# Optimization experiments

Measured on AMD Instinct MI355X. Metric: run time of the kernel, lower is better.

Reference implementation:

```python
import jax, jax.numpy as jnp
import numpy as np

N_NODES = 100000
N_EDGES = 1280000
IN_DIM = 64
HID = 64
OUT_DIM = 2
N_GRAPHS = 1000
BN_EPS = 1e-5


def setup_inputs() -> dict:
    key = jax.random.key(0)
    ks = jax.random.split(key, 16)
    x = jax.random.normal(ks[0], (N_NODES, IN_DIM), dtype=jnp.float32)
    edge_index = jax.random.randint(ks[1], (2, N_EDGES), 0, N_NODES, dtype=jnp.int64)
    batch = jnp.sort(jax.random.randint(ks[2], (N_NODES,), 0, N_GRAPHS, dtype=jnp.int64))
    # He-init linear weights (stored as [in, out] so forward is x @ W)
    def he(k, fan_in, fan_out):
        return jax.random.normal(k, (fan_in, fan_out), dtype=jnp.float32) * np.sqrt(2.0 / fan_in)
    return {
        "x": x,
        "edge_index": edge_index,
        "batch": batch,
        "bn_in_g": jnp.ones((IN_DIM,), jnp.float32),
        "bn_in_b": jnp.zeros((IN_DIM,), jnp.float32),
        "W1": he(ks[3], IN_DIM, HID), "b1": jnp.zeros((HID,), jnp.float32),
        "g1": jnp.ones((HID,), jnp.float32), "be1": jnp.zeros((HID,), jnp.float32),
        "W2": he(ks[4], HID, HID), "b2": jnp.zeros((HID,), jnp.float32),
        "g2": jnp.ones((HID,), jnp.float32), "be2": jnp.zeros((HID,), jnp.float32),
        "Wout": he(ks[5], HID, OUT_DIM), "bout": jnp.zeros((OUT_DIM,), jnp.float32),
    }


def _batchnorm(x, g, b):
    # training-mode BN over the node dimension (biased variance, as torch uses for normalization)
    m = jnp.mean(x, axis=0)
    v = jnp.mean(jnp.square(x - m), axis=0)
    return (x - m) * jax.lax.rsqrt(v + BN_EPS) * g + b


def _gcn_norm(edge_index, n):
    # PyG GCNConv normalization with added self-loops:
    # norm_e = deg[src]^-1/2 * deg[dst]^-1/2, deg computed on A + I over targets.
    row = jnp.concatenate([edge_index[0], jnp.arange(n, dtype=edge_index.dtype)])
    col = jnp.concatenate([edge_index[1], jnp.arange(n, dtype=edge_index.dtype)])
    deg = jax.ops.segment_sum(jnp.ones_like(col, dtype=jnp.float32), col, num_segments=n)
    dinv = jnp.where(deg > 0, jax.lax.rsqrt(deg), 0.0)
    norm = dinv[row] * dinv[col]
    return row, col, norm


def _gcn_conv(x, W, b, row, col, norm, n):
    h = x @ W                                   # [N, out]
    msg = h[row] * norm[:, None]                # gather over edges (incl. self-loops)
    agg = jax.ops.segment_sum(msg, col, num_segments=n)
    return agg + b


def reference(x, edge_index, batch, bn_in_g, bn_in_b, W1, b1, g1, be1, W2, b2, g2, be2, Wout, bout):
    n = x.shape[0]
    row, col, norm = _gcn_norm(edge_index, n)
    h = _batchnorm(x, bn_in_g, bn_in_b)         # input BN (dropout = identity in eval)
    h = _gcn_conv(h, W1, b1, row, col, norm, n)
    h = _batchnorm(jax.nn.relu(h), g1, be1)
    h = _gcn_conv(h, W2, b2, row, col, norm, n)
    h = _batchnorm(jax.nn.relu(h), g2, be2)
    # global mean pool per graph
    sums = jax.ops.segment_sum(h, batch, num_segments=N_GRAPHS)
    cnts = jax.ops.segment_sum(jnp.ones((n,), h.dtype), batch, num_segments=N_GRAPHS)
    pooled = sums / jnp.maximum(cnts, 1.0)[:, None]
    return pooled @ Wout + bout                 # [N_GRAPHS, OUT_DIM]
```

## Files before the change

### kernel.cpp

```cpp
#include <hip/hip_runtime.h>
#include <math.h>

#define N_NODES 100000
#define N_EDGES 1280000
#define DIM 64
#define N_GRAPHS 1000
#define BN_EPS 1e-5f
#define NB 392
#define P1B 256
#define P1E 5000
#define SB 400
#define WIN 128
#define NWIN (N_EDGES / WIN)
#define GU 8
#define NSLOT 32

__device__ __forceinline__ unsigned int bf16_rtn2(float a, float b) {
    unsigned int ua = __float_as_uint(a);
    unsigned int ub = __float_as_uint(b);
    ua = (ua + 0x7FFFu + ((ua >> 16) & 1u)) >> 16;
    ub = (ub + 0x7FFFu + ((ub >> 16) & 1u)) >> 16;
    return ua | (ub << 16);
}
__device__ __forceinline__ unsigned short bf16r(float a) {
    unsigned int u = __float_as_uint(a);
    return (unsigned short)((u + 0x7FFFu + ((u >> 16) & 1u)) >> 16);
}
__device__ __forceinline__ float bfup(unsigned short u) {
    return __uint_as_float(((unsigned int)u) << 16);
}

__global__ __launch_bounds__(256) void k_p1hist(const int* __restrict__ ei,
                                                const int* __restrict__ batch,
                                                const float* __restrict__ X,
                                                int* __restrict__ bh,
                                                int* __restrict__ start,
                                                float* __restrict__ gsum,
                                                float* __restrict__ gsumsq) {
    int t = threadIdx.x;
    if (blockIdx.x < P1B) {
        __shared__ int hist[NB];
        for (int b = t; b < NB; b += 256) hist[b] = 0;
        __syncthreads();
        int e0 = blockIdx.x * P1E;
        #pragma unroll 4
        for (int e = e0 + t; e < e0 + P1E; e += 256)
            atomicAdd(&hist[ei[N_EDGES + e] >> 8], 1);
        __syncthreads();
        for (int b = t; b < NB; b += 256) bh[b * P1B + blockIdx.x] = hist[b];
    } else if (blockIdx.x < P1B + SB) {
        int grp = blockIdx.x - P1B;
        int j = t & 63, rg = t >> 6;
        int base = grp * 250;
        float s = 0.f, s2 = 0.f;
        for (int i = base + rg; i < base + 250; i += 4) {
            float v = X[i * DIM + j];
            s += v; s2 += v * v;
        }
        __shared__ float ls[256], ls2[256];
        ls[t] = s; ls2[t] = s2;
        __syncthreads();
        if (t < 64) {
            int slot = (grp & (NSLOT - 1)) * DIM;
            s  = ls[j]  + ls[64 + j]  + ls[128 + j]  + ls[192 + j];
            s2 = ls2[j] + ls2[64 + j] + ls2[128 + j] + ls2[192 + j];
            atomicAdd(&gsum[slot + j], s);
            atomicAdd(&gsumsq[slot + j], s2);
        }
    } else {
        int i = (blockIdx.x - P1B - SB) * 256 + t;
        if (i < N_NODES) {
            int cur = batch[i];
            if (i == 0) { for (int q = 0; q <= cur; q++) start[q] = 0; }
            else {
                int prev = batch[i - 1];
                for (int q = prev + 1; q <= cur; q++) start[q] = i;
            }
            if (i == N_NODES - 1)
                for (int q = cur + 1; q <= N_GRAPHS; q++) start[q] = N_NODES;
        }
    }
}

__global__ void k_scan1(const int* __restrict__ bh, int* __restrict__ iscan,
                        int* __restrict__ bsum) {
    __shared__ int ls[256];
    int i = blockIdx.x * 256 + threadIdx.x;
    int v = bh[i];
    ls[threadIdx.x] = v;
    __syncthreads();
    for (int off = 1; off < 256; off <<= 1) {
        int tv = (threadIdx.x >= off) ? ls[threadIdx.x - off] : 0;
        __syncthreads();
        ls[threadIdx.x] += tv;
        __syncthreads();
    }
    iscan[i] = ls[threadIdx.x];
    if (threadIdx.x == 255) bsum[blockIdx.x] = ls[255];
}

__global__ void k_scan2(const int* __restrict__ bsum, int* __restrict__ boff) {
    __shared__ int ls[512];
    int t = threadIdx.x;
    int v0 = (t < NB) ? bsum[t] : 0;
    ls[t] = v0;
    __syncthreads();
    for (int off = 1; off < 512; off <<= 1) {
        int v = (t >= off) ? ls[t - off] : 0;
        __syncthreads();
        ls[t] += v;
        __syncthreads();
    }
    if (t < NB) boff[t] = ls[t] - v0;
}

__global__ __launch_bounds__(256) void k_p1scat(const int* __restrict__ ei,
                                                const int* __restrict__ bh,
                                                const int* __restrict__ iscan,
                                                const int* __restrict__ boff,
                                                int2* __restrict__ tmp) {
    __shared__ int cur[NB];
    int blk = blockIdx.x;
    for (int b = threadIdx.x; b < NB; b += 256) {
        int i = b * P1B + blk;
        cur[b] = boff[b] + iscan[i] - bh[i];
    }
    __syncthreads();
    int e0 = blk * P1E;
    for (int e = e0 + threadIdx.x; e < e0 + P1E; e += 256) {
        int r = ei[e], c = ei[N_EDGES + e];
        int pos = atomicAdd(&cur[c >> 8], 1);
        tmp[pos] = make_int2(r, c);
    }
}

__global__ __launch_bounds__(256) void k_p2a(const int2* __restrict__ tmp,
                                             const int* __restrict__ bh,
                                             const int* __restrict__ iscan,
                                             const int* __restrict__ boff,
                                             int* __restrict__ rowstart,
                                             float* __restrict__ dinv,
                                             int* __restrict__ winnode) {
    int b = blockIdx.x, t = threadIdx.x;
    int bstart = boff[b] + iscan[b * 256] - bh[b * 256];
    int bend = (b == NB - 1) ? N_EDGES
                             : (boff[b + 1] + iscan[(b + 1) * 256] - bh[(b + 1) * 256]);
    __shared__ int cnt[256], scn[256];
    cnt[t] = 0;
    __syncthreads();
    for (int e = bstart + t; e < bend; e += 256)
        atomicAdd(&cnt[tmp[e].y & 255], 1);
    __syncthreads();
    scn[t] = cnt[t];
    __syncthreads();
    for (int off = 1; off < 256; off <<= 1) {
        int v = (t >= off) ? scn[t - off] : 0;
        __syncthreads();
        scn[t] += v;
        __syncthreads();
    }
    int node = b * 256 + t;
    int rs = bstart + scn[t] - cnt[t];
    if (node <= N_NODES) rowstart[node] = rs;
    if (node < N_NODES) {
        int deg = cnt[t];
        dinv[node] = 1.0f / sqrtf((float)(deg + 1));
        int re = rs + deg;
        for (int w = (rs + WIN - 1) / WIN; w * WIN < re; ++w) winnode[w] = node;
    }
}

__global__ __launch_bounds__(256) void k_p2b(const int2* __restrict__ tmp,
                                             const int* __restrict__ bh,
                                             const int* __restrict__ iscan,
                                             const int* __restrict__ boff,
                                             const int* __restrict__ rowstart,
                                             const float* __restrict__ dinv,
                                             int2* __restrict__ csr_ew) {
    int b = blockIdx.x, t = threadIdx.x;
    int bstart = boff[b] + iscan[b * 256] - bh[b * 256];
    int bend = (b == NB - 1) ? N_EDGES
                             : (boff[b + 1] + iscan[(b + 1) * 256] - bh[(b + 1) * 256]);
    __shared__ int curs[256];
    __shared__ float dl[256];
    int node = b * 256 + t;
    curs[t] = (node < N_NODES) ? rowstart[node] : 0;
    dl[t]   = (node < N_NODES) ? dinv[node] : 0.f;
    __syncthreads();
    for (int e = bstart + t; e < bend; e += 256) {
        int2 rec = tmp[e];
        int ld = rec.y & 255;
        int pos = atomicAdd(&curs[ld], 1);
        float w = dl[ld] * dinv[rec.x];
        csr_ew[pos] = make_int2(rec.x, (int)__float_as_uint(w));
    }
}

__global__ void k_bnfold(float* __restrict__ gsum, float* __restrict__ gsumsq,
                         const float* __restrict__ g, const float* __restrict__ b,
                         const float* __restrict__ W,
                         float* __restrict__ scale, float* __restrict__ cshift) {
    int j = threadIdx.x;
    float ms = 0.f, m2 = 0.f;
    for (int k = 0; k < NSLOT; k++) {
        ms += gsum[k * DIM + j];   gsum[k * DIM + j] = 0.f;
        m2 += gsumsq[k * DIM + j]; gsumsq[k * DIM + j] = 0.f;
    }
    float mean = ms * (1.0f / N_NODES);
    float var  = m2 * (1.0f / N_NODES) - mean * mean;
    float inv  = 1.0f / sqrtf(var + BN_EPS);
    float sc   = g[j] * inv;
    scale[j] = sc;
    __shared__ float shl[64];
    shl[j] = b[j] - mean * sc;
    __syncthreads();
    float s = 0.f;
    for (int k = 0; k < DIM; k++) s += shl[k] * W[k * DIM + j];
    cshift[j] = s;
}

__global__ void k_bnfinal(const float* __restrict__ gsum, const float* __restrict__ gsumsq,
                          const float* __restrict__ g, const float* __restrict__ b,
                          float* __restrict__ scale, float* __restrict__ shift) {
    int j = threadIdx.x;
    float ms = 0.f, m2 = 0.f;
    for (int k = 0; k < NSLOT; k++) { ms += gsum[k * DIM + j]; m2 += gsumsq[k * DIM + j]; }
    float mean = ms * (1.0f / N_NODES);
    float var  = m2 * (1.0f / N_NODES) - mean * mean;
    float inv  = 1.0f / sqrtf(var + BN_EPS);
    float sc   = g[j] * inv;
    scale[j] = sc;
    shift[j] = b[j] - mean * sc;
}

__global__ __launch_bounds__(256) void k_gemm_f32(const float* __restrict__ X,
                                                  const float* __restrict__ W,
                                                  const float* __restrict__ scale,
                                                  const float* __restrict__ cshift,
                                                  unsigned short* __restrict__ T) {
    __shared__ float Wl[64 * 64];
    __shared__ float Al[64 * 65];
    for (int t = threadIdx.x; t < 4096; t += 256) {
        int k = t >> 6;
        Wl[t] = W[t] * scale[k];
    }
    int row0 = blockIdx.x * 64;
    for (int t = threadIdx.x; t < 4096; t += 256) {
        int r = t >> 6, k = t & 63;
        int i = row0 + r;
        Al[r * 65 + k] = (i < N_NODES) ? X[(size_t)i * DIM + k] : 0.f;
    }
    __syncthreads();
    int r = threadIdx.x & 63;
    int q = threadIdx.x >> 6;
    float acc[16];
    #pragma unroll
    for (int jj = 0; jj < 16; jj++) acc[jj] = cshift[q * 16 + jj];
    #pragma unroll 4
    for (int k = 0; k < 64; k++) {
        float a = Al[r * 65 + k];
        const float4* wv = (const float4*)&Wl[k * 64 + q * 16];
        float4 w0 = wv[0], w1 = wv[1], w2 = wv[2], w3 = wv[3];
        acc[0]  += a * w0.x; acc[1]  += a * w0.y; acc[2]  += a * w0.z; acc[3]  += a * w0.w;
        acc[4]  += a * w1.x; acc[5]  += a * w1.y; acc[6]  += a * w1.z; acc[7]  += a * w1.w;
        acc[8]  += a * w2.x; acc[9]  += a * w2.y; acc[10] += a * w2.z; acc[11] += a * w2.w;
        acc[12] += a * w3.x; acc[13] += a * w3.y; acc[14] += a * w3.z; acc[15] += a * w3.w;
    }
    int i = row0 + r;
    if (i < N_NODES) {
        unsigned int pk[8];
        #pragma unroll
        for (int jj = 0; jj < 8; jj++) pk[jj] = bf16_rtn2(acc[2 * jj], acc[2 * jj + 1]);
        uint4* outv = (uint4*)&T[(size_t)i * DIM + q * 16];
        outv[0] = make_uint4(pk[0], pk[1], pk[2], pk[3]);
        outv[1] = make_uint4(pk[4], pk[5], pk[6], pk[7]);
    }
}

__global__ __launch_bounds__(256) void k_gemm_b16(const unsigned short* __restrict__ X,
                                                  const float* __restrict__ W,
                                                  const float* __restrict__ scale,
                                                  const float* __restrict__ cshift,
                                                  unsigned short* __restrict__ T) {
    __shared__ float Wl[64 * 64];
    __shared__ float Al[64 * 65];
    for (int t = threadIdx.x; t < 4096; t += 256) {
        int k = t >> 6;
        Wl[t] = W[t] * scale[k];
    }
    int row0 = blockIdx.x * 64;
    for (int t = threadIdx.x; t < 4096; t += 256) {
        int r = t >> 6, k = t & 63;
        int i = row0 + r;
        Al[r * 65 + k] = (i < N_NODES) ? bfup(X[(size_t)i * DIM + k]) : 0.f;
    }
    __syncthreads();
    int r = threadIdx.x & 63;
    int q = threadIdx.x >> 6;
    float acc[16];
    #pragma unroll
    for (int jj = 0; jj < 16; jj++) acc[jj] = cshift[q * 16 + jj];
    #pragma unroll 4
    for (int k = 0; k < 64; k++) {
        float a = Al[r * 65 + k];
        const float4* wv = (const float4*)&Wl[k * 64 + q * 16];
        float4 w0 = wv[0], w1 = wv[1], w2 = wv[2], w3 = wv[3];
        acc[0]  += a * w0.x; acc[1]  += a * w0.y; acc[2]  += a * w0.z; acc[3]  += a * w0.w;
        acc[4]  += a * w1.x; acc[5]  += a * w1.y; acc[6]  += a * w1.z; acc[7]  += a * w1.w;
        acc[8]  += a * w2.x; acc[9]  += a * w2.y; acc[10] += a * w2.z; acc[11] += a * w2.w;
        acc[12] += a * w3.x; acc[13] += a * w3.y; acc[14] += a * w3.z; acc[15] += a * w3.w;
    }
    int i = row0 + r;
    if (i < N_NODES) {
        unsigned int pk[8];
        #pragma unroll
        for (int jj = 0; jj < 8; jj++) pk[jj] = bf16_rtn2(acc[2 * jj], acc[2 * jj + 1]);
        uint4* outv = (uint4*)&T[(size_t)i * DIM + q * 16];
        outv[0] = make_uint4(pk[0], pk[1], pk[2], pk[3]);
        outv[1] = make_uint4(pk[4], pk[5], pk[6], pk[7]);
    }
}

__global__ __launch_bounds__(256) void k_zstrad(const int* __restrict__ rowstart,
                                                const int* __restrict__ winnode,
                                                float* __restrict__ C) {
    int lane = threadIdx.x & 63;
    int w = blockIdx.x * 4 + (threadIdx.x >> 6);
    int n = winnode[w];
    if (rowstart[n] < w * WIN)
        C[(size_t)n * DIM + lane] = 0.f;
}

__global__ __launch_bounds__(256) void k_gather1(const unsigned short* __restrict__ T,
                                                 const float* __restrict__ dinv,
                                                 const int* __restrict__ rowstart,
                                                 const int* __restrict__ winnode,
                                                 const int2* __restrict__ csr_ew,
                                                 const float* __restrict__ bias,
                                                 float* __restrict__ C,
                                                 unsigned short* __restrict__ H,
                                                 float* __restrict__ gsum,
                                                 float* __restrict__ gsumsq) {
    int lane = threadIdx.x & 63;
    int w = blockIdx.x * 4 + (threadIdx.x >> 6);
    float bb = bias[lane];
    float s = 0.f, s2 = 0.f;
    int e = w * WIN;
    const int eend = e + WIN;
    int i  = __builtin_amdgcn_readfirstlane(winnode[w]);
    int re = __builtin_amdgcn_readfirstlane(rowstart[i + 1]);
    bool part = __builtin_amdgcn_readfirstlane(rowstart[i]) < e;
    float acc = 0.f;
    for (; e < eend; e += GU) {
        int src[GU]; float wt[GU];
        int eu = __builtin_amdgcn_readfirstlane(e);
        #pragma unroll
        for (int u = 0; u < GU; u++) {
            int2 ew = csr_ew[eu + u];
            src[u] = ew.x; wt[u] = __uint_as_float((unsigned int)ew.y);
        }
        float tv[GU];
        #pragma unroll
        for (int u = 0; u < GU; u++) tv[u] = bfup(T[(size_t)src[u] * DIM + lane]);
        #pragma unroll
        for (int u = 0; u < GU; u++) {
            while (e + u == re) {
                if (part) { atomicAdd(&C[(size_t)i * DIM + lane], acc); part = false; }
                else {
                    float di = dinv[i];
                    float h = fmaxf(acc + bfup(T[(size_t)i * DIM + lane]) * (di * di) + bb, 0.f);
                    H[(size_t)i * DIM + lane] = bf16r(h);
                    s += h; s2 += h * h;
                }
                acc = 0.f; ++i;
                re = __builtin_amdgcn_readfirstlane(rowstart[i + 1]);
            }
            acc += tv[u] * wt[u];
        }
    }
    if (part || re > eend) atomicAdd(&C[(size_t)i * DIM + lane], acc);
    else {
        float di = dinv[i];
        float h = fmaxf(acc + bfup(T[(size_t)i * DIM + lane]) * (di * di) + bb, 0.f);
        H[(size_t)i * DIM + lane] = bf16r(h);
        s += h; s2 += h * h;
    }
    __shared__ float ls[256], ls2[256];
    ls[threadIdx.x] = s; ls2[threadIdx.x] = s2;
    __syncthreads();
    if (threadIdx.x < 64) {
        int j = threadIdx.x;
        int slot = (blockIdx.x & (NSLOT - 1)) * DIM;
        atomicAdd(&gsum[slot + j],   ls[j] + ls[64 + j] + ls[128 + j] + ls[192 + j]);
        atomicAdd(&gsumsq[slot + j], ls2[j] + ls2[64 + j] + ls2[128 + j] + ls2[192 + j]);
    }
}

__global__ __launch_bounds__(256) void k_gather2(const unsigned short* __restrict__ T,
                                                 const float* __restrict__ dinv,
                                                 const int* __restrict__ rowstart,
                                                 const int* __restrict__ winnode,
                                                 const int2* __restrict__ csr_ew,
                                                 const float* __restrict__ bias,
                                                 const int* __restrict__ batch,
                                                 float* __restrict__ C,
                                                 float* __restrict__ pool,
                                                 float* __restrict__ gsum,
                                                 float* __restrict__ gsumsq) {
    int lane = threadIdx.x & 63;
    int w = blockIdx.x * 4 + (threadIdx.x >> 6);
    float bb = bias[lane];
    float s = 0.f, s2 = 0.f, ps = 0.f;
    int cur_g = -1;
    int e = w * WIN;
    const int eend = e + WIN;
    int i  = __builtin_amdgcn_readfirstlane(winnode[w]);
    int re = __builtin_amdgcn_readfirstlane(rowstart[i + 1]);
    bool part = __builtin_amdgcn_readfirstlane(rowstart[i]) < e;
    float acc = 0.f;
    for (; e < eend; e += GU) {
        int src[GU]; float wt[GU];
        int eu = __builtin_amdgcn_readfirstlane(e);
        #pragma unroll
        for (int u = 0; u < GU; u++) {
            int2 ew = csr_ew[eu + u];
            src[u] = ew.x; wt[u] = __uint_as_float((unsigned int)ew.y);
        }
        float tv[GU];
        #pragma unroll
        for (int u = 0; u < GU; u++) tv[u] = bfup(T[(size_t)src[u] * DIM + lane]);
        #pragma unroll
        for (int u = 0; u < GU; u++) {
            while (e + u == re) {
                if (part) { atomicAdd(&C[(size_t)i * DIM + lane], acc); part = false; }
                else {
                    float di = dinv[i];
                    float h = fmaxf(acc + bfup(T[(size_t)i * DIM + lane]) * (di * di) + bb, 0.f);
                    s += h; s2 += h * h;
                    int g = batch[i];
                    if (g != cur_g) {
                        if (cur_g >= 0) atomicAdd(&pool[(size_t)cur_g * DIM + lane], ps);
                        ps = 0.f; cur_g = g;
                    }
                    ps += h;
                }
                acc = 0.f; ++i;
                re = __builtin_amdgcn_readfirstlane(rowstart[i + 1]);
            }
            acc += tv[u] * wt[u];
        }
    }
    if (part || re > eend) atomicAdd(&C[(size_t)i * DIM + lane], acc);
    else {
        float di = dinv[i];
        float h = fmaxf(acc + bfup(T[(size_t)i * DIM + lane]) * (di * di) + bb, 0.f);
        s += h; s2 += h * h;
        int g = batch[i];
        if (g != cur_g) {
            if (cur_g >= 0) atomicAdd(&pool[(size_t)cur_g * DIM + lane], ps);
            ps = 0.f; cur_g = g;
        }
        ps += h;
    }
    if (cur_g >= 0) atomicAdd(&pool[(size_t)cur_g * DIM + lane], ps);
    __shared__ float ls[256], ls2[256];
    ls[threadIdx.x] = s; ls2[threadIdx.x] = s2;
    __syncthreads();
    if (threadIdx.x < 64) {
        int j = threadIdx.x;
        int slot = (blockIdx.x & (NSLOT - 1)) * DIM;
        atomicAdd(&gsum[slot + j],   ls[j] + ls[64 + j] + ls[128 + j] + ls[192 + j]);
        atomicAdd(&gsumsq[slot + j], ls2[j] + ls2[64 + j] + ls2[128 + j] + ls2[192 + j]);
    }
}

__global__ __launch_bounds__(256) void k_strad1(const float* __restrict__ C,
                                                const unsigned short* __restrict__ T,
                                                const float* __restrict__ dinv,
                                                const int* __restrict__ rowstart,
                                                const int* __restrict__ winnode,
                                                const float* __restrict__ bias,
                                                unsigned short* __restrict__ H,
                                                float* __restrict__ gsum,
                                                float* __restrict__ gsumsq) {
    int lane = threadIdx.x & 63;
    int wv = threadIdx.x >> 6;
    float bb = bias[lane];
    float s = 0.f, s2 = 0.f;
    __shared__ int anyw;
    if (threadIdx.x == 0) anyw = 0;
    __syncthreads();
    if (blockIdx.x < NWIN / 4) {
        int w = blockIdx.x * 4 + wv;
        int n = winnode[w];
        int rs = rowstart[n];
        if (w == rs / WIN + 1) {
            float di = dinv[n];
            float h = fmaxf(C[(size_t)n * DIM + lane]
                            + bfup(T[(size_t)n * DIM + lane]) * (di * di) + bb, 0.f);
            H[(size_t)n * DIM + lane] = bf16r(h);
            s += h; s2 += h * h;
            anyw = 1;
        }
    } else {
        int base = (blockIdx.x - NWIN / 4) * 256 + wv * 64;
        int nb = base + lane;
        int d0 = 0;
        if (nb < N_NODES)
            d0 = (rowstart[nb + 1] == rowstart[nb]) && ((rowstart[nb] & (WIN - 1)) == 0);
        unsigned long long m = __ballot(d0);
        while (m) {
            int b = __builtin_ctzll(m);
            m &= m - 1;
            int n = base + b;
            float di = dinv[n];
            float h = fmaxf(bfup(T[(size_t)n * DIM + lane]) * (di * di) + bb, 0.f);
            H[(size_t)n * DIM + lane] = bf16r(h);
            s += h; s2 += h * h;
            anyw = 1;
        }
    }
    __shared__ float ls[256], ls2[256];
    ls[threadIdx.x] = s; ls2[threadIdx.x] = s2;
    __syncthreads();
    if (anyw && threadIdx.x < 64) {
        int j = threadIdx.x;
        int slot = (blockIdx.x & (NSLOT - 1)) * DIM;
        atomicAdd(&gsum[slot + j],   ls[j] + ls[64 + j] + ls[128 + j] + ls[192 + j]);
        atomicAdd(&gsumsq[slot + j], ls2[j] + ls2[64 + j] + ls2[128 + j] + ls2[192 + j]);
    }
}

__global__ __launch_bounds__(256) void k_strad2(const float* __restrict__ C,
                                                const unsigned short* __restrict__ T,
                                                const float* __restrict__ dinv,
                                                const int* __restrict__ rowstart,
                                                const int* __restrict__ winnode,
                                                const float* __restrict__ bias,
                                                const int* __restrict__ batch,
                                                float* __restrict__ pool,
                                                float* __restrict__ gsum,
                                                float* __restrict__ gsumsq) {
    int lane = threadIdx.x & 63;
    int wv = threadIdx.x >> 6;
    float bb = bias[lane];
    float s = 0.f, s2 = 0.f;
    __shared__ int anyw;
    if (threadIdx.x == 0) anyw = 0;
    __syncthreads();
    if (blockIdx.x < NWIN / 4) {
        int w = blockIdx.x * 4 + wv;
        int n = winnode[w];
        int rs = rowstart[n];
        if (w == rs / WIN + 1) {
            float di = dinv[n];
            float h = fmaxf(C[(size_t)n * DIM + lane]
                            + bfup(T[(size_t)n * DIM + lane]) * (di * di) + bb, 0.f);
            s += h; s2 += h * h;
            atomicAdd(&pool[(size_t)batch[n] * DIM + lane], h);
            anyw = 1;
        }
    } else {
        int base = (blockIdx.x - NWIN / 4) * 256 + wv * 64;
        int nb = base + lane;
        int d0 = 0;
        if (nb < N_NODES)
            d0 = (rowstart[nb + 1] == rowstart[nb]) && ((rowstart[nb] & (WIN - 1)) == 0);
        unsigned long long m = __ballot(d0);
        while (m) {
            int b = __builtin_ctzll(m);
            m &= m - 1;
            int n = base + b;
            float di = dinv[n];
            float h = fmaxf(bfup(T[(size_t)n * DIM + lane]) * (di * di) + bb, 0.f);
            s += h; s2 += h * h;
            atomicAdd(&pool[(size_t)batch[n] * DIM + lane], h);
            anyw = 1;
        }
    }
    __shared__ float ls[256], ls2[256];
    ls[threadIdx.x] = s; ls2[threadIdx.x] = s2;
    __syncthreads();
    if (anyw && threadIdx.x < 64) {
        int j = threadIdx.x;
        int slot = (blockIdx.x & (NSLOT - 1)) * DIM;
        atomicAdd(&gsum[slot + j],   ls[j] + ls[64 + j] + ls[128 + j] + ls[192 + j]);
        atomicAdd(&gsumsq[slot + j], ls2[j] + ls2[64 + j] + ls2[128 + j] + ls2[192 + j]);
    }
}

__global__ void k_final(const float* __restrict__ pool, const int* __restrict__ start,
                        const float* __restrict__ scale, const float* __restrict__ shift,
                        const float* __restrict__ Wout, const float* __restrict__ bout,
                        float* __restrict__ out) {
    int g = blockIdx.x;
    int l = threadIdx.x;
    float c = fmaxf((float)(start[g + 1] - start[g]), 1.f);
    float p = (pool[g * DIM + l] / c) * scale[l] + shift[l];
    float a0 = p * Wout[l * 2 + 0];
    float a1 = p * Wout[l * 2 + 1];
    #pragma unroll
    for (int off = 32; off; off >>= 1) {
        a0 += __shfl_down(a0, off, 64);
        a1 += __shfl_down(a1, off, 64);
    }
    if (l == 0) {
        out[g * 2 + 0] = a0 + bout[0];
        out[g * 2 + 1] = a1 + bout[1];
    }
}

extern "C" void kernel_launch(void* const* d_in, const int* in_sizes, int n_in,
                              void* d_out, int out_size, void* d_ws, size_t ws_size,
                              hipStream_t stream) {
    (void)in_sizes; (void)n_in; (void)out_size; (void)ws_size;
    const float* x       = (const float*)d_in[0];
    const int*   ei      = (const int*)d_in[1];
    const int*   batch   = (const int*)d_in[2];
    const float* bn_in_g = (const float*)d_in[3];
    const float* bn_in_b = (const float*)d_in[4];
    const float* W1      = (const float*)d_in[5];
    const float* b1      = (const float*)d_in[6];
    const float* g1      = (const float*)d_in[7];
    const float* be1     = (const float*)d_in[8];
    const float* W2      = (const float*)d_in[9];
    const float* b2      = (const float*)d_in[10];
    const float* g2      = (const float*)d_in[11];
    const float* be2     = (const float*)d_in[12];
    const float* Wout    = (const float*)d_in[13];
    const float* bout    = (const float*)d_in[14];
    float* out = (float*)d_out;

    char* p = (char*)d_ws;
    float* C = (float*)p;                   p += (size_t)N_NODES * DIM * 4;
    unsigned short* H = (unsigned short*)p; p += (size_t)N_NODES * DIM * 2;
    unsigned short* T = (unsigned short*)p; p += (size_t)N_NODES * DIM * 2;
    int2* csr_ew = (int2*)p;                p += (size_t)N_EDGES * 8;
    float* dinv = (float*)p;                p += N_NODES * 4;
    int* bh = (int*)p;                      p += NB * P1B * 4;
    int* iscan = (int*)p;                   p += NB * P1B * 4;
    int* rowstart = (int*)p;                p += (N_NODES + 2) * 4;
    int* winnode = (int*)p;                 p += NWIN * 4;
    int* bsum = (int*)p;                    p += NB * 4;
    int* boff = (int*)p;                    p += NB * 4;
    int* start = (int*)p;                   p += (N_GRAPHS + 2) * 4;
    float* gsum = (float*)p;                p += NSLOT * DIM * 4;
    float* gsumsq = (float*)p;              p += NSLOT * DIM * 4;
    float* scale = (float*)p;               p += DIM * 4;
    float* shift = (float*)p;               p += DIM * 4;
    float* cshift = (float*)p;              p += DIM * 4;
    float* pool = (float*)p;                p += (size_t)N_GRAPHS * DIM * 4;
    int2* tmp = (int2*)H;

    hipMemsetAsync(gsum, 0, 2 * NSLOT * DIM * sizeof(float), stream);
    hipMemsetAsync(pool, 0, (size_t)N_GRAPHS * DIM * sizeof(float), stream);
    k_p1hist<<<P1B + SB + 392, 256, 0, stream>>>(ei, batch, x, bh, start, gsum, gsumsq);
    k_scan1<<<NB, 256, 0, stream>>>(bh, iscan, bsum);
    k_scan2<<<1, 512, 0, stream>>>(bsum, boff);
    k_p1scat<<<P1B, 256, 0, stream>>>(ei, bh, iscan, boff, tmp);
    k_p2a<<<NB, 256, 0, stream>>>(tmp, bh, iscan, boff, rowstart, dinv, winnode);
    k_p2b<<<NB, 256, 0, stream>>>(tmp, bh, iscan, boff, rowstart, dinv, csr_ew);

    k_bnfold<<<1, 64, 0, stream>>>(gsum, gsumsq, bn_in_g, bn_in_b, W1, scale, cshift);
    k_gemm_f32<<<(N_NODES + 63) / 64, 256, 0, stream>>>(x, W1, scale, cshift, T);
    k_zstrad<<<NWIN / 4, 256, 0, stream>>>(rowstart, winnode, C);
    k_gather1<<<NWIN / 4, 256, 0, stream>>>(T, dinv, rowstart, winnode, csr_ew, b1,
                                            C, H, gsum, gsumsq);
    k_strad1<<<NWIN / 4 + 392, 256, 0, stream>>>(C, T, dinv, rowstart, winnode, b1,
                                                 H, gsum, gsumsq);

    k_bnfold<<<1, 64, 0, stream>>>(gsum, gsumsq, g1, be1, W2, scale, cshift);
    k_gemm_b16<<<(N_NODES + 63) / 64, 256, 0, stream>>>(H, W2, scale, cshift, T);
    k_zstrad<<<NWIN / 4, 256, 0, stream>>>(rowstart, winnode, C);
    k_gather2<<<NWIN / 4, 256, 0, stream>>>(T, dinv, rowstart, winnode, csr_ew, b2,
                                            batch, C, pool, gsum, gsumsq);
    k_strad2<<<NWIN / 4 + 392, 256, 0, stream>>>(C, T, dinv, rowstart, winnode, b2,
                                                 batch, pool, gsum, gsumsq);

    k_bnfinal<<<1, 64, 0, stream>>>(gsum, gsumsq, g2, be2, scale, shift);
    k_final<<<N_GRAPHS, 64, 0, stream>>>(pool, start, scale, shift, Wout, bout, out);
}
```

Measured before the change: 353.4 us.

## Fuse preprocessing and BN-fold kernels, drop edge weights, compact straddle node list

```diff
diff --git a/kernel.cpp b/kernel.cpp
--- a/kernel.cpp
+++ b/kernel.cpp
@@ -14,6 +14,8 @@
 #define NWIN (N_EDGES / WIN)
 #define GU 8
 #define NSLOT 32
+#define NG ((N_NODES + 63) / 64)
+#define ZB 625
 
 __device__ __forceinline__ unsigned int bf16_rtn2(float a, float b) {
     unsigned int ua = __float_as_uint(a);
@@ -82,43 +84,50 @@
     }
 }
 
-__global__ void k_scan1(const int* __restrict__ bh, int* __restrict__ iscan,
-                        int* __restrict__ bsum) {
+__global__ __launch_bounds__(256) void k_scan12(const int* __restrict__ bh,
+                                                int* __restrict__ iscan,
+                                                int* __restrict__ bsum,
+                                                int* __restrict__ boff,
+                                                int* __restrict__ ctr) {
     __shared__ int ls[256];
-    int i = blockIdx.x * 256 + threadIdx.x;
-    int v = bh[i];
-    ls[threadIdx.x] = v;
+    int t = threadIdx.x;
+    int i = blockIdx.x * 256 + t;
+    ls[t] = bh[i];
     __syncthreads();
     for (int off = 1; off < 256; off <<= 1) {
-        int tv = (threadIdx.x >= off) ? ls[threadIdx.x - off] : 0;
-        __syncthreads();
-        ls[threadIdx.x] += tv;
-        __syncthreads();
-    }
-    iscan[i] = ls[threadIdx.x];
-    if (threadIdx.x == 255) bsum[blockIdx.x] = ls[255];
-}
-
-__global__ void k_scan2(const int* __restrict__ bsum, int* __restrict__ boff) {
-    __shared__ int ls[512];
-    int t = threadIdx.x;
-    int v0 = (t < NB) ? bsum[t] : 0;
-    ls[t] = v0;
+        int v = (t >= off) ? ls[t - off] : 0;
+        __syncthreads();
+        ls[t] += v;
+        __syncthreads();
+    }
+    iscan[i] = ls[t];
+    if (t == 255) bsum[blockIdx.x] = ls[255];
+    __threadfence();
+    __shared__ int isLast;
+    if (t == 0) isLast = (atomicAdd(ctr, 1) == NB - 1);
+    __syncthreads();
+    if (!isLast) return;
+    __shared__ int l2[512];
+    int a0 = (t < NB) ? atomicAdd(&bsum[t], 0) : 0;
+    int a1 = (t + 256 < NB) ? atomicAdd(&bsum[t + 256], 0) : 0;
+    l2[t] = a0; l2[t + 256] = a1;
     __syncthreads();
     for (int off = 1; off < 512; off <<= 1) {
-        int v = (t >= off) ? ls[t - off] : 0;
-        __syncthreads();
-        ls[t] += v;
-        __syncthreads();
-    }
-    if (t < NB) boff[t] = ls[t] - v0;
+        int v1 = (t >= off) ? l2[t - off] : 0;
+        int v2 = l2[t + 256 - off];
+        __syncthreads();
+        l2[t] += v1; l2[t + 256] += v2;
+        __syncthreads();
+    }
+    if (t < NB) boff[t] = l2[t] - a0;
+    if (t + 256 < NB) boff[t + 256] = l2[t + 256] - a1;
 }
 
 __global__ __launch_bounds__(256) void k_p1scat(const int* __restrict__ ei,
                                                 const int* __restrict__ bh,
                                                 const int* __restrict__ iscan,
                                                 const int* __restrict__ boff,
-                                                int2* __restrict__ tmp) {
+                                                int* __restrict__ tmp) {
     __shared__ int cur[NB];
     int blk = blockIdx.x;
     for (int b = threadIdx.x; b < NB; b += 256) {
@@ -130,26 +139,29 @@
     for (int e = e0 + threadIdx.x; e < e0 + P1E; e += 256) {
         int r = ei[e], c = ei[N_EDGES + e];
         int pos = atomicAdd(&cur[c >> 8], 1);
-        tmp[pos] = make_int2(r, c);
-    }
-}
-
-__global__ __launch_bounds__(256) void k_p2a(const int2* __restrict__ tmp,
-                                             const int* __restrict__ bh,
-                                             const int* __restrict__ iscan,
-                                             const int* __restrict__ boff,
-                                             int* __restrict__ rowstart,
-                                             float* __restrict__ dinv,
-                                             int* __restrict__ winnode) {
+        tmp[pos] = (r << 8) | (c & 255);
+    }
+}
+
+__global__ __launch_bounds__(256) void k_p2ab(const int* __restrict__ tmp,
+                                              const int* __restrict__ bh,
+                                              const int* __restrict__ iscan,
+                                              const int* __restrict__ boff,
+                                              int* __restrict__ rowstart,
+                                              float* __restrict__ dinv,
+                                              int* __restrict__ winnode,
+                                              int* __restrict__ csr,
+                                              int* __restrict__ slist,
+                                              int* __restrict__ scnt) {
     int b = blockIdx.x, t = threadIdx.x;
     int bstart = boff[b] + iscan[b * 256] - bh[b * 256];
     int bend = (b == NB - 1) ? N_EDGES
                              : (boff[b + 1] + iscan[(b + 1) * 256] - bh[(b + 1) * 256]);
-    __shared__ int cnt[256], scn[256];
+    __shared__ int cnt[256], scn[256], curs[256];
     cnt[t] = 0;
     __syncthreads();
     for (int e = bstart + t; e < bend; e += 256)
-        atomicAdd(&cnt[tmp[e].y & 255], 1);
+        atomicAdd(&cnt[tmp[e] & 255], 1);
     __syncthreads();
     scn[t] = cnt[t];
     __syncthreads();
@@ -160,102 +172,84 @@
         __syncthreads();
     }
     int node = b * 256 + t;
-    int rs = bstart + scn[t] - cnt[t];
-    if (node <= N_NODES) rowstart[node] = rs;
+    int deg = cnt[t];
+    int rs = bstart + scn[t] - deg;
     if (node < N_NODES) {
-        int deg = cnt[t];
+        rowstart[node] = rs;
         dinv[node] = 1.0f / sqrtf((float)(deg + 1));
         int re = rs + deg;
         for (int w = (rs + WIN - 1) / WIN; w * WIN < re; ++w) winnode[w] = node;
-    }
-}
-
-__global__ __launch_bounds__(256) void k_p2b(const int2* __restrict__ tmp,
-                                             const int* __restrict__ bh,
-                                             const int* __restrict__ iscan,
-                                             const int* __restrict__ boff,
-                                             const int* __restrict__ rowstart,
-                                             const float* __restrict__ dinv,
-                                             int2* __restrict__ csr_ew) {
-    int b = blockIdx.x, t = threadIdx.x;
-    int bstart = boff[b] + iscan[b * 256] - bh[b * 256];
-    int bend = (b == NB - 1) ? N_EDGES
-                             : (boff[b + 1] + iscan[(b + 1) * 256] - bh[(b + 1) * 256]);
-    __shared__ int curs[256];
-    __shared__ float dl[256];
-    int node = b * 256 + t;
-    curs[t] = (node < N_NODES) ? rowstart[node] : 0;
-    dl[t]   = (node < N_NODES) ? dinv[node] : 0.f;
+        bool span = (deg > 0) && (rs / WIN != (re - 1) / WIN);
+        bool z0 = (deg == 0) && ((rs & (WIN - 1)) == 0);
+        if (span || z0) {
+            int p = atomicAdd(scnt, 1);
+            slist[p] = z0 ? (node | 0x40000000) : node;
+        }
+    }
+    if (b == 0 && t == 0) rowstart[N_NODES] = N_EDGES;
+    curs[t] = rs;
     __syncthreads();
     for (int e = bstart + t; e < bend; e += 256) {
-        int2 rec = tmp[e];
-        int ld = rec.y & 255;
-        int pos = atomicAdd(&curs[ld], 1);
-        float w = dl[ld] * dinv[rec.x];
-        csr_ew[pos] = make_int2(rec.x, (int)__float_as_uint(w));
-    }
-}
-
-__global__ void k_bnfold(float* __restrict__ gsum, float* __restrict__ gsumsq,
-                         const float* __restrict__ g, const float* __restrict__ b,
-                         const float* __restrict__ W,
-                         float* __restrict__ scale, float* __restrict__ cshift) {
-    int j = threadIdx.x;
-    float ms = 0.f, m2 = 0.f;
-    for (int k = 0; k < NSLOT; k++) {
-        ms += gsum[k * DIM + j];   gsum[k * DIM + j] = 0.f;
-        m2 += gsumsq[k * DIM + j]; gsumsq[k * DIM + j] = 0.f;
-    }
-    float mean = ms * (1.0f / N_NODES);
-    float var  = m2 * (1.0f / N_NODES) - mean * mean;
-    float inv  = 1.0f / sqrtf(var + BN_EPS);
-    float sc   = g[j] * inv;
-    scale[j] = sc;
-    __shared__ float shl[64];
-    shl[j] = b[j] - mean * sc;
-    __syncthreads();
-    float s = 0.f;
-    for (int k = 0; k < DIM; k++) s += shl[k] * W[k * DIM + j];
-    cshift[j] = s;
-}
-
-__global__ void k_bnfinal(const float* __restrict__ gsum, const float* __restrict__ gsumsq,
-                          const float* __restrict__ g, const float* __restrict__ b,
-                          float* __restrict__ scale, float* __restrict__ shift) {
-    int j = threadIdx.x;
-    float ms = 0.f, m2 = 0.f;
-    for (int k = 0; k < NSLOT; k++) { ms += gsum[k * DIM + j]; m2 += gsumsq[k * DIM + j]; }
-    float mean = ms * (1.0f / N_NODES);
-    float var  = m2 * (1.0f / N_NODES) - mean * mean;
-    float inv  = 1.0f / sqrtf(var + BN_EPS);
-    float sc   = g[j] * inv;
-    scale[j] = sc;
-    shift[j] = b[j] - mean * sc;
-}
-
-__global__ __launch_bounds__(256) void k_gemm_f32(const float* __restrict__ X,
-                                                  const float* __restrict__ W,
-                                                  const float* __restrict__ scale,
-                                                  const float* __restrict__ cshift,
-                                                  unsigned short* __restrict__ T) {
+        int rec = tmp[e];
+        int pos = atomicAdd(&curs[rec & 255], 1);
+        csr[pos] = (int)((unsigned)rec >> 8);
+    }
+}
+
+__global__ __launch_bounds__(256) void k_gemm1(const float* __restrict__ X,
+                                               const float* __restrict__ W,
+                                               const float* __restrict__ gv,
+                                               const float* __restrict__ bv,
+                                               const float* __restrict__ gsum,
+                                               const float* __restrict__ gsumsq,
+                                               const float* __restrict__ dinv,
+                                               const int* __restrict__ rowstart,
+                                               const int* __restrict__ winnode,
+                                               float* __restrict__ C,
+                                               unsigned short* __restrict__ T) {
+    int t = threadIdx.x;
+    if (blockIdx.x >= NG) {
+        int lane = t & 63;
+        int wb = (blockIdx.x - NG) * 16 + (t >> 6) * 4;
+        #pragma unroll
+        for (int k = 0; k < 4; k++) {
+            int w = wb + k;
+            int n = winnode[w];
+            if (rowstart[n] < w * WIN) C[(size_t)n * DIM + lane] = 0.f;
+        }
+        return;
+    }
     __shared__ float Wl[64 * 64];
     __shared__ float Al[64 * 65];
-    for (int t = threadIdx.x; t < 4096; t += 256) {
-        int k = t >> 6;
-        Wl[t] = W[t] * scale[k];
+    __shared__ float scl[64], shl[64], csh[64];
+    if (t < 64) {
+        float ms = 0.f, m2 = 0.f;
+        for (int k = 0; k < NSLOT; k++) { ms += gsum[k * DIM + t]; m2 += gsumsq[k * DIM + t]; }
+        float mean = ms * (1.0f / N_NODES);
+        float var  = m2 * (1.0f / N_NODES) - mean * mean;
+        float inv  = 1.0f / sqrtf(var + BN_EPS);
+        float sc   = gv[t] * inv;
+        scl[t] = sc;
+        shl[t] = bv[t] - mean * sc;
+    }
+    __syncthreads();
+    for (int i = t; i < 4096; i += 256) Wl[i] = W[i] * scl[i >> 6];
+    if (t < 64) {
+        float s = 0.f;
+        for (int k = 0; k < 64; k++) s += shl[k] * W[k * 64 + t];
+        csh[t] = s;
     }
     int row0 = blockIdx.x * 64;
-    for (int t = threadIdx.x; t < 4096; t += 256) {
-        int r = t >> 6, k = t & 63;
-        int i = row0 + r;
-        Al[r * 65 + k] = (i < N_NODES) ? X[(size_t)i * DIM + k] : 0.f;
-    }
-    __syncthreads();
-    int r = threadIdx.x & 63;
-    int q = threadIdx.x >> 6;
+    for (int i = t; i < 4096; i += 256) {
+        int r = i >> 6, k = i & 63;
+        int n = row0 + r;
+        Al[r * 65 + k] = (n < N_NODES) ? X[(size_t)n * DIM + k] : 0.f;
+    }
+    __syncthreads();
+    int r = t & 63, q = t >> 6;
     float acc[16];
     #pragma unroll
-    for (int jj = 0; jj < 16; jj++) acc[jj] = cshift[q * 16 + jj];
+    for (int jj = 0; jj < 16; jj++) acc[jj] = csh[q * 16 + jj];
     #pragma unroll 4
     for (int k = 0; k < 64; k++) {
         float a = Al[r * 65 + k];
@@ -268,38 +262,71 @@
     }
     int i = row0 + r;
     if (i < N_NODES) {
+        float dv = dinv[i];
         unsigned int pk[8];
         #pragma unroll
-        for (int jj = 0; jj < 8; jj++) pk[jj] = bf16_rtn2(acc[2 * jj], acc[2 * jj + 1]);
+        for (int jj = 0; jj < 8; jj++)
+            pk[jj] = bf16_rtn2(acc[2 * jj] * dv, acc[2 * jj + 1] * dv);
         uint4* outv = (uint4*)&T[(size_t)i * DIM + q * 16];
         outv[0] = make_uint4(pk[0], pk[1], pk[2], pk[3]);
         outv[1] = make_uint4(pk[4], pk[5], pk[6], pk[7]);
     }
 }
 
-__global__ __launch_bounds__(256) void k_gemm_b16(const unsigned short* __restrict__ X,
-                                                  const float* __restrict__ W,
-                                                  const float* __restrict__ scale,
-                                                  const float* __restrict__ cshift,
-                                                  unsigned short* __restrict__ T) {
+__global__ __launch_bounds__(256) void k_gemm2(const unsigned short* __restrict__ X,
+                                               const float* __restrict__ W,
+                                               const float* __restrict__ gv,
+                                               const float* __restrict__ bv,
+                                               const float* __restrict__ gsum,
+                                               const float* __restrict__ gsumsq,
+                                               const float* __restrict__ dinv,
+                                               const int* __restrict__ rowstart,
+                                               const int* __restrict__ winnode,
+                                               float* __restrict__ C,
+                                               unsigned short* __restrict__ T) {
+    int t = threadIdx.x;
+    if (blockIdx.x >= NG) {
+        int lane = t & 63;
+        int wb = (blockIdx.x - NG) * 16 + (t >> 6) * 4;
+        #pragma unroll
+        for (int k = 0; k < 4; k++) {
+            int w = wb + k;
+            int n = winnode[w];
+            if (rowstart[n] < w * WIN) C[(size_t)n * DIM + lane] = 0.f;
+        }
+        return;
+    }
     __shared__ float Wl[64 * 64];
     __shared__ float Al[64 * 65];
-    for (int t = threadIdx.x; t < 4096; t += 256) {
-        int k = t >> 6;
-        Wl[t] = W[t] * scale[k];
+    __shared__ float scl[64], shl[64], csh[64];
+    if (t < 64) {
+        float ms = 0.f, m2 = 0.f;
+        for (int k = 0; k < NSLOT; k++) { ms += gsum[k * DIM + t]; m2 += gsumsq[k * DIM + t]; }
+        float mean = ms * (1.0f / N_NODES);
+        float var  = m2 * (1.0f / N_NODES) - mean * mean;
+        float inv  = 1.0f / sqrtf(var + BN_EPS);
+        float sc   = gv[t] * inv;
+        scl[t] = sc;
+        shl[t] = bv[t] - mean * sc;
+    }
+    __syncthreads();
+    for (int i = t; i < 4096; i += 256) Wl[i] = W[i] * scl[i >> 6];
+    if (t < 64) {
+        float s = 0.f;
+        for (int k = 0; k < 64; k++) s += shl[k] * W[k * 64 + t];
+        csh[t] = s;
     }
     int row0 = blockIdx.x * 64;
-    for (int t = threadIdx.x; t < 4096; t += 256) {
-        int r = t >> 6, k = t & 63;
-        int i = row0 + r;
-        Al[r * 65 + k] = (i < N_NODES) ? bfup(X[(size_t)i * DIM + k]) : 0.f;
-    }
-    __syncthreads();
-    int r = threadIdx.x & 63;
-    int q = threadIdx.x >> 6;
+    for (int i = t; i < 4096; i += 256) {
+        int r = i >> 6, k = i & 63;
+        int n = row0 + r;
+        Al[r * 65 + k] = (n < N_NODES) ? bfup(X[(size_t)n * DIM + k]) : 0.f;
+    }
+    __syncthreads();
+    int r = t & 63, q = t >> 6;
     float acc[16];
     #pragma unroll
-    for (int jj = 0; jj < 16; jj++) acc[jj] = cshift[q * 16 + jj];
+    for (int jj = 0; jj < 16; jj++) acc[jj] = csh[q * 16 + jj];
     #pragma unroll 4
     for (int k = 0; k < 64; k++) {
         float a = Al[r * 65 + k];
@@ -312,30 +339,22 @@
     }
     int i = row0 + r;
     if (i < N_NODES) {
+        float dv = dinv[i];
         unsigned int pk[8];
         #pragma unroll
-        for (int jj = 0; jj < 8; jj++) pk[jj] = bf16_rtn2(acc[2 * jj], acc[2 * jj + 1]);
+        for (int jj = 0; jj < 8; jj++)
+            pk[jj] = bf16_rtn2(acc[2 * jj] * dv, acc[2 * jj + 1] * dv);
         uint4* outv = (uint4*)&T[(size_t)i * DIM + q * 16];
         outv[0] = make_uint4(pk[0], pk[1], pk[2], pk[3]);
         outv[1] = make_uint4(pk[4], pk[5], pk[6], pk[7]);
     }
-}
-
-__global__ __launch_bounds__(256) void k_zstrad(const int* __restrict__ rowstart,
-                                                const int* __restrict__ winnode,
-                                                float* __restrict__ C) {
-    int lane = threadIdx.x & 63;
-    int w = blockIdx.x * 4 + (threadIdx.x >> 6);
-    int n = winnode[w];
-    if (rowstart[n] < w * WIN)
-        C[(size_t)n * DIM + lane] = 0.f;
 }
 
 __global__ __launch_bounds__(256) void k_gather1(const unsigned short* __restrict__ T,
                                                  const float* __restrict__ dinv,
                                                  const int* __restrict__ rowstart,
                                                  const int* __restrict__ winnode,
-                                                 const int2* __restrict__ csr_ew,
+                                                 const int* __restrict__ csr,
                                                  const float* __restrict__ bias,
                                                  float* __restrict__ C,
                                                  unsigned short* __restrict__ H,
@@ -352,13 +371,10 @@
     bool part = __builtin_amdgcn_readfirstlane(rowstart[i]) < e;
     float acc = 0.f;
     for (; e < eend; e += GU) {
-        int src[GU]; float wt[GU];
+        int src[GU];
         int eu = __builtin_amdgcn_readfirstlane(e);
         #pragma unroll
-        for (int u = 0; u < GU; u++) {
-            int2 ew = csr_ew[eu + u];
-            src[u] = ew.x; wt[u] = __uint_as_float((unsigned int)ew.y);
-        }
+        for (int u = 0; u < GU; u++) src[u] = csr[eu + u];
         float tv[GU];
         #pragma unroll
         for (int u = 0; u < GU; u++) tv[u] = bfup(T[(size_t)src[u] * DIM + lane]);
@@ -368,20 +384,20 @@
                 if (part) { atomicAdd(&C[(size_t)i * DIM + lane], acc); part = false; }
                 else {
                     float di = dinv[i];
-                    float h = fmaxf(acc + bfup(T[(size_t)i * DIM + lane]) * (di * di) + bb, 0.f);
+                    float h = fmaxf((acc + bfup(T[(size_t)i * DIM + lane])) * di + bb, 0.f);
                     H[(size_t)i * DIM + lane] = bf16r(h);
                     s += h; s2 += h * h;
                 }
                 acc = 0.f; ++i;
                 re = __builtin_amdgcn_readfirstlane(rowstart[i + 1]);
             }
-            acc += tv[u] * wt[u];
+            acc += tv[u];
         }
     }
     if (part || re > eend) atomicAdd(&C[(size_t)i * DIM + lane], acc);
     else {
         float di = dinv[i];
-        float h = fmaxf(acc + bfup(T[(size_t)i * DIM + lane]) * (di * di) + bb, 0.f);
+        float h = fmaxf((acc + bfup(T[(size_t)i * DIM + lane])) * di + bb, 0.f);
         H[(size_t)i * DIM + lane] = bf16r(h);
         s += h; s2 += h * h;
     }
@@ -400,7 +416,7 @@
                                                  const float* __restrict__ dinv,
                                                  const int* __restrict__ rowstart,
                                                  const int* __restrict__ winnode,
-                                                 const int2* __restrict__ csr_ew,
+                                                 const int* __restrict__ csr,
                                                  const float* __restrict__ bias,
                                                  const int* __restrict__ batch,
                                                  float* __restrict__ C,
@@ -419,13 +435,10 @@
     bool part = __builtin_amdgcn_readfirstlane(rowstart[i]) < e;
     float acc = 0.f;
     for (; e < eend; e += GU) {
-        int src[GU]; float wt[GU];
+        int src[GU];
         int eu = __builtin_amdgcn_readfirstlane(e);
         #pragma unroll
-        for (int u = 0; u < GU; u++) {
-            int2 ew = csr_ew[eu + u];
-            src[u] = ew.x; wt[u] = __uint_as_float((unsigned int)ew.y);
-        }
+        for (int u = 0; u < GU; u++) src[u] = csr[eu + u];
         float tv[GU];
         #pragma unroll
         for (int u = 0; u < GU; u++) tv[u] = bfup(T[(size_t)src[u] * DIM + lane]);
@@ -435,7 +448,7 @@
                 if (part) { atomicAdd(&C[(size_t)i * DIM + lane], acc); part = false; }
                 else {
                     float di = dinv[i];
-                    float h = fmaxf(acc + bfup(T[(size_t)i * DIM + lane]) * (di * di) + bb, 0.f);
+                    float h = fmaxf((acc + bfup(T[(size_t)i * DIM + lane])) * di + bb, 0.f);
                     s += h; s2 += h * h;
                     int g = batch[i];
                     if (g != cur_g) {
@@ -447,13 +460,13 @@
                 acc = 0.f; ++i;
                 re = __builtin_amdgcn_readfirstlane(rowstart[i + 1]);
             }
-            acc += tv[u] * wt[u];
+            acc += tv[u];
         }
     }
     if (part || re > eend) atomicAdd(&C[(size_t)i * DIM + lane], acc);
     else {
         float di = dinv[i];
-        float h = fmaxf(acc + bfup(T[(size_t)i * DIM + lane]) * (di * di) + bb, 0.f);
+        float h = fmaxf((acc + bfup(T[(size_t)i * DIM + lane])) * di + bb, 0.f);
         s += h; s2 += h * h;
         int g = batch[i];
         if (g != cur_g) {
@@ -477,53 +490,29 @@
 __global__ __launch_bounds__(256) void k_strad1(const float* __restrict__ C,
                                                 const unsigned short* __restrict__ T,
                                                 const float* __restrict__ dinv,
-                                                const int* __restrict__ rowstart,
-                                                const int* __restrict__ winnode,
+                                                const int* __restrict__ slist,
+                                                const int* __restrict__ scnt,
                                                 const float* __restrict__ bias,
                                                 unsigned short* __restrict__ H,
                                                 float* __restrict__ gsum,
                                                 float* __restrict__ gsumsq) {
-    int lane = threadIdx.x & 63;
-    int wv = threadIdx.x >> 6;
+    int lane = threadIdx.x & 63, wv = threadIdx.x >> 6;
     float bb = bias[lane];
     float s = 0.f, s2 = 0.f;
-    __shared__ int anyw;
-    if (threadIdx.x == 0) anyw = 0;
-    __syncthreads();
-    if (blockIdx.x < NWIN / 4) {
-        int w = blockIdx.x * 4 + wv;
-        int n = winnode[w];
-        int rs = rowstart[n];
-        if (w == rs / WIN + 1) {
-            float di = dinv[n];
-            float h = fmaxf(C[(size_t)n * DIM + lane]
-                            + bfup(T[(size_t)n * DIM + lane]) * (di * di) + bb, 0.f);
-            H[(size_t)n * DIM + lane] = bf16r(h);
-            s += h; s2 += h * h;
-            anyw = 1;
-        }
-    } else {
-        int base = (blockIdx.x - NWIN / 4) * 256 + wv * 64;
-        int nb = base + lane;
-        int d0 = 0;
-        if (nb < N_NODES)
-            d0 = (rowstart[nb + 1] == rowstart[nb]) && ((rowstart[nb] & (WIN - 1)) == 0);
-        unsigned long long m = __ballot(d0);
-        while (m) {
-            int b = __builtin_ctzll(m);
-            m &= m - 1;
-            int n = base + b;
-            float di = dinv[n];
-            float h = fmaxf(bfup(T[(size_t)n * DIM + lane]) * (di * di) + bb, 0.f);
-            H[(size_t)n * DIM + lane] = bf16r(h);
-            s += h; s2 += h * h;
-            anyw = 1;
-        }
+    int n_items = scnt[0];
+    for (int idx = blockIdx.x * 4 + wv; idx < n_items; idx += gridDim.x * 4) {
+        int rec = slist[idx];
+        int n = rec & 0x3FFFFFFF;
+        float c = (rec & 0x40000000) ? 0.f : C[(size_t)n * DIM + lane];
+        float di = dinv[n];
+        float h = fmaxf((c + bfup(T[(size_t)n * DIM + lane])) * di + bb, 0.f);
+        H[(size_t)n * DIM + lane] = bf16r(h);
+        s += h; s2 += h * h;
     }
     __shared__ float ls[256], ls2[256];
     ls[threadIdx.x] = s; ls2[threadIdx.x] = s2;
     __syncthreads();
-    if (anyw && threadIdx.x < 64) {
+    if (threadIdx.x < 64) {
         int j = threadIdx.x;
         int slot = (blockIdx.x & (NSLOT - 1)) * DIM;
         atomicAdd(&gsum[slot + j],   ls[j] + ls[64 + j] + ls[128 + j] + ls[192 + j]);
@@ -534,54 +523,30 @@
 __global__ __launch_bounds__(256) void k_strad2(const float* __restrict__ C,
                                                 const unsigned short* __restrict__ T,
                                                 const float* __restrict__ dinv,
-                                                const int* __restrict__ rowstart,
-                                                const int* __restrict__ winnode,
+                                                const int* __restrict__ slist,
+                                                const int* __restrict__ scnt,
                                                 const float* __restrict__ bias,
                                                 const int* __restrict__ batch,
                                                 float* __restrict__ pool,
                                                 float* __restrict__ gsum,
                                                 float* __restrict__ gsumsq) {
-    int lane = threadIdx.x & 63;
-    int wv = threadIdx.x >> 6;
+    int lane = threadIdx.x & 63, wv = threadIdx.x >> 6;
     float bb = bias[lane];
     float s = 0.f, s2 = 0.f;
-    __shared__ int anyw;
-    if (threadIdx.x == 0) anyw = 0;
-    __syncthreads();
-    if (blockIdx.x < NWIN / 4) {
-        int w = blockIdx.x * 4 + wv;
-        int n = winnode[w];
-        int rs = rowstart[n];
-        if (w == rs / WIN + 1) {
-            float di = dinv[n];
-            float h = fmaxf(C[(size_t)n * DIM + lane]
-                            + bfup(T[(size_t)n * DIM + lane]) * (di * di) + bb, 0.f);
-            s += h; s2 += h * h;
-            atomicAdd(&pool[(size_t)batch[n] * DIM + lane], h);
-            anyw = 1;
-        }
-    } else {
-        int base = (blockIdx.x - NWIN / 4) * 256 + wv * 64;
-        int nb = base + lane;
-        int d0 = 0;
-        if (nb < N_NODES)
-            d0 = (rowstart[nb + 1] == rowstart[nb]) && ((rowstart[nb] & (WIN - 1)) == 0);
-        unsigned long long m = __ballot(d0);
-        while (m) {
-            int b = __builtin_ctzll(m);
-            m &= m - 1;
-            int n = base + b;
-            float di = dinv[n];
-            float h = fmaxf(bfup(T[(size_t)n * DIM + lane]) * (di * di) + bb, 0.f);
-            s += h; s2 += h * h;
-            atomicAdd(&pool[(size_t)batch[n] * DIM + lane], h);
-            anyw = 1;
-        }
+    int n_items = scnt[0];
+    for (int idx = blockIdx.x * 4 + wv; idx < n_items; idx += gridDim.x * 4) {
+        int rec = slist[idx];
+        int n = rec & 0x3FFFFFFF;
+        float c = (rec & 0x40000000) ? 0.f : C[(size_t)n * DIM + lane];
+        float di = dinv[n];
+        float h = fmaxf((c + bfup(T[(size_t)n * DIM + lane])) * di + bb, 0.f);
+        s += h; s2 += h * h;
+        atomicAdd(&pool[(size_t)batch[n] * DIM + lane], h);
     }
     __shared__ float ls[256], ls2[256];
     ls[threadIdx.x] = s; ls2[threadIdx.x] = s2;
     __syncthreads();
-    if (anyw && threadIdx.x < 64) {
+    if (threadIdx.x < 64) {
         int j = threadIdx.x;
         int slot = (blockIdx.x & (NSLOT - 1)) * DIM;
         atomicAdd(&gsum[slot + j],   ls[j] + ls[64 + j] + ls[128 + j] + ls[192 + j]);
@@ -590,13 +555,21 @@
 }
 
 __global__ void k_final(const float* __restrict__ pool, const int* __restrict__ start,
-                        const float* __restrict__ scale, const float* __restrict__ shift,
+                        const float* __restrict__ gsum, const float* __restrict__ gsumsq,
+                        const float* __restrict__ gv, const float* __restrict__ bv,
                         const float* __restrict__ Wout, const float* __restrict__ bout,
                         float* __restrict__ out) {
     int g = blockIdx.x;
     int l = threadIdx.x;
+    float ms = 0.f, m2 = 0.f;
+    for (int k = 0; k < NSLOT; k++) { ms += gsum[k * DIM + l]; m2 += gsumsq[k * DIM + l]; }
+    float mean = ms * (1.0f / N_NODES);
+    float var  = m2 * (1.0f / N_NODES) - mean * mean;
+    float inv  = 1.0f / sqrtf(var + BN_EPS);
+    float sc   = gv[l] * inv;
+    float sh   = bv[l] - mean * sc;
     float c = fmaxf((float)(start[g + 1] - start[g]), 1.f);
-    float p = (pool[g * DIM + l] / c) * scale[l] + shift[l];
+    float p = (pool[g * DIM + l] / c) * sc + sh;
     float a0 = p * Wout[l * 2 + 0];
     float a1 = p * Wout[l * 2 + 1];
     #pragma unroll
@@ -635,7 +608,7 @@
     float* C = (float*)p;                   p += (size_t)N_NODES * DIM * 4;
     unsigned short* H = (unsigned short*)p; p += (size_t)N_NODES * DIM * 2;
     unsigned short* T = (unsigned short*)p; p += (size_t)N_NODES * DIM * 2;
-    int2* csr_ew = (int2*)p;                p += (size_t)N_EDGES * 8;
+    int* csr = (int*)p;                     p += (size_t)N_EDGES * 4;
     float* dinv = (float*)p;                p += N_NODES * 4;
     int* bh = (int*)p;                      p += NB * P1B * 4;
     int* iscan = (int*)p;                   p += NB * P1B * 4;
@@ -644,39 +617,41 @@
     int* bsum = (int*)p;                    p += NB * 4;
     int* boff = (int*)p;                    p += NB * 4;
     int* start = (int*)p;                   p += (N_GRAPHS + 2) * 4;
-    float* gsum = (float*)p;                p += NSLOT * DIM * 4;
-    float* gsumsq = (float*)p;              p += NSLOT * DIM * 4;
-    float* scale = (float*)p;               p += DIM * 4;
-    float* shift = (float*)p;               p += DIM * 4;
-    float* cshift = (float*)p;              p += DIM * 4;
+    int* slist = (int*)p;                   p += N_NODES * 4;
+    char* zbase = p;
+    int* scnt = (int*)p;                    p += 4;
+    int* ctr = (int*)p;                     p += 4;
+    p += 8;
+    float* gsum0 = (float*)p;               p += NSLOT * DIM * 4;
+    float* gsumsq0 = (float*)p;             p += NSLOT * DIM * 4;
+    float* gsum1 = (float*)p;               p += NSLOT * DIM * 4;
+    float* gsumsq1 = (float*)p;             p += NSLOT * DIM * 4;
+    float* gsum2 = (float*)p;               p += NSLOT * DIM * 4;
+    float* gsumsq2 = (float*)p;             p += NSLOT * DIM * 4;
     float* pool = (float*)p;                p += (size_t)N_GRAPHS * DIM * 4;
-    int2* tmp = (int2*)H;
-
-    hipMemsetAsync(gsum, 0, 2 * NSLOT * DIM * sizeof(float), stream);
-    hipMemsetAsync(pool, 0, (size_t)N_GRAPHS * DIM * sizeof(float), stream);
-    k_p1hist<<<P1B + SB + 392, 256, 0, stream>>>(ei, batch, x, bh, start, gsum, gsumsq);
-    k_scan1<<<NB, 256, 0, stream>>>(bh, iscan, bsum);
-    k_scan2<<<1, 512, 0, stream>>>(bsum, boff);
+    size_t zbytes = (size_t)(p - zbase);
+    int* tmp = (int*)H;
+
+    hipMemsetAsync(zbase, 0, zbytes, stream);
+    k_p1hist<<<P1B + SB + 392, 256, 0, stream>>>(ei, batch, x, bh, start, gsum0, gsumsq0);
+    k_scan12<<<NB, 256, 0, stream>>>(bh, iscan, bsum, boff, ctr);
     k_p1scat<<<P1B, 256, 0, stream>>>(ei, bh, iscan, boff, tmp);
-    k_p2a<<<NB, 256, 0, stream>>>(tmp, bh, iscan, boff, rowstart, dinv, winnode);
-    k_p2b<<<NB, 256, 0, stream>>>(tmp, bh, iscan, boff, rowstart, dinv, csr_ew);
-
-    k_bnfold<<<1, 64, 0, stream>>>(gsum, gsumsq, bn_in_g, bn_in_b, W1, scale, cshift);
-    k_gemm_f32<<<(N_NODES + 63) / 64, 256, 0, stream>>>(x, W1, scale, cshift, T);
-    k_zstrad<<<NWIN / 4, 256, 0, stream>>>(rowstart, winnode, C);
-    k_gather1<<<NWIN / 4, 256, 0, stream>>>(T, dinv, rowstart, winnode, csr_ew, b1,
-                                            C, H, gsum, gsumsq);
-    k_strad1<<<NWIN / 4 + 392, 256, 0, stream>>>(C, T, dinv, rowstart, winnode, b1,
-                                                 H, gsum, gsumsq);
-
-    k_bnfold<<<1, 64, 0, stream>>>(gsum, gsumsq, g1, be1, W2, scale, cshift);
-    k_gemm_b16<<<(N_NODES + 63) / 64, 256, 0, stream>>>(H, W2, scale, cshift, T);
-    k_zstrad<<<NWIN / 4, 256, 0, stream>>>(rowstart, winnode, C);
-    k_gather2<<<NWIN / 4, 256, 0, stream>>>(T, dinv, rowstart, winnode, csr_ew, b2,
-                                            batch, C, pool, gsum, gsumsq);
-    k_strad2<<<NWIN / 4 + 392, 256, 0, stream>>>(C, T, dinv, rowstart, winnode, b2,
-                                                 batch, pool, gsum, gsumsq);
-
-    k_bnfinal<<<1, 64, 0, stream>>>(gsum, gsumsq, g2, be2, scale, shift);
-    k_final<<<N_GRAPHS, 64, 0, stream>>>(pool, start, scale, shift, Wout, bout, out);
-}
+    k_p2ab<<<NB, 256, 0, stream>>>(tmp, bh, iscan, boff, rowstart, dinv, winnode,
+                                   csr, slist, scnt);
+
+    k_gemm1<<<NG + ZB, 256, 0, stream>>>(x, W1, bn_in_g, bn_in_b, gsum0, gsumsq0,
+                                         dinv, rowstart, winnode, C, T);
+    k_gather1<<<NWIN / 4, 256, 0, stream>>>(T, dinv, rowstart, winnode, csr, b1,
+                                            C, H, gsum1, gsumsq1);
+    k_strad1<<<64, 256, 0, stream>>>(C, T, dinv, slist, scnt, b1, H, gsum1, gsumsq1);
+
+    k_gemm2<<<NG + ZB, 256, 0, stream>>>(H, W2, g1, be1, gsum1, gsumsq1,
+                                         dinv, rowstart, winnode, C, T);
+    k_gather2<<<NWIN / 4, 256, 0, stream>>>(T, dinv, rowstart, winnode, csr, b2,
+                                            batch, C, pool, gsum2, gsumsq2);
+    k_strad2<<<64, 256, 0, stream>>>(C, T, dinv, slist, scnt, b2, batch, pool,
+                                     gsum2, gsumsq2);
+
+    k_final<<<N_GRAPHS, 64, 0, stream>>>(pool, start, gsum2, gsumsq2, g2, be2,
+                                         Wout, bout, out);
+}
```

Measured after the change: 403.5 us. 14.2% more time.
